# Kernel tuning notes

Measured on AMD Instinct MI355X. Metric: run time of the kernel, lower is better.

Reference implementation:

```python
import jax, jax.numpy as jnp
import numpy as np

B, S, DIN, DIM = 4, 4096, 256, 256
GAMMA = 0.9865


def setup_inputs() -> dict:
    key = jax.random.key(0)
    ks = jax.random.split(key, 9)
    inp = {
        'xq': jax.random.normal(ks[0], (B, S, DIN), dtype=jnp.float32),
        'xk': jax.random.normal(ks[1], (B, S, DIN), dtype=jnp.float32),
        'xv': jax.random.normal(ks[2], (B, S, DIN), dtype=jnp.float32),
        'Wq': jax.random.normal(ks[3], (DIN, DIM), dtype=jnp.float32) * 0.05,
        'bq': jnp.zeros((DIM,), dtype=jnp.float32),
        'Wk': jax.random.normal(ks[4], (DIN, DIM), dtype=jnp.float32) * 0.05,
        'bk': jnp.zeros((DIM,), dtype=jnp.float32),
        'Wv': jax.random.normal(ks[5], (DIN, DIM), dtype=jnp.float32) * 0.05,
        'bv': jnp.zeros((DIM,), dtype=jnp.float32),
    }
    return inp


def _decay_matrix(s, gamma):
    # D[i, j] = gamma^(i-j) if i >= j else 0
    idx = jnp.arange(s)
    diff = idx[:, None] - idx[None, :]
    D = jnp.where(diff >= 0,
                  jnp.power(jnp.float32(gamma), diff.astype(jnp.float32)),
                  jnp.float32(0.0))
    return D


def reference(xq, xk, xv, Wq, bq, Wk, bk, Wv, bv):
    Q = xq @ Wq + bq  # [B,S,D]
    K = xk @ Wk + bk  # [B,S,D]
    V = xv @ Wv + bv  # [B,S,D]
    d = Q.shape[-1]
    # scores[b,i,j] = Q[b,i] . K[b,j] / sqrt(d)
    x = jnp.einsum('bid,bjd->bij', Q, K) / jnp.sqrt(jnp.float32(d))
    D = _decay_matrix(S, GAMMA)
    # Faithful to TF broadcasting: divides along the LAST axis (per-column by
    # sqrt of that index's row-sum): D[i,j] /= sqrt(sum_k D[j,k])
    D = D / jnp.sqrt(jnp.sum(D, axis=-1))
    x = x * D  # broadcast [B,S,S] * [S,S]
    # _norm_3 per batch element with TF broadcasting: x[b,i,j] /= max(|sum_k x[b,j,k]|, 1)
    denom = jnp.maximum(jnp.abs(jnp.sum(x, axis=-1)), 1.0)  # [B,S]
    x = x / denom[:, None, :]
    return x @ V  # [B,S,D]
```

## Files before the change

### kernel.cpp

```cpp
#include <hip/hip_runtime.h>
#include <math.h>

#define BB 4
#define SS 4096
#define DD 256
#define LL 256
#define NCH 16
#define GAMMA 0.9865f
#define LOG2G (-0.019609034f)
#define INV1MG 74.07407407f
#define SLAB 1032
#define SLABB 520

typedef __attribute__((ext_vector_type(8))) short short8;
typedef __attribute__((ext_vector_type(4))) float f32x4;
typedef unsigned short u16;
typedef unsigned int u32;

__device__ __forceinline__ u16 f2bf(float f) {
  union { float f; unsigned u; } v; v.f = f;
  unsigned r = v.u + 0x7FFFu + ((v.u >> 16) & 1u);
  return (u16)(r >> 16);
}
__device__ __forceinline__ float bf2f(u16 h) {
  union { unsigned u; float f; } v; v.u = ((unsigned)h) << 16; return v.f;
}

__device__ __forceinline__ void gll16(const u16* g, u16* l) {
  __builtin_amdgcn_global_load_lds(
      (const __attribute__((address_space(1))) u32*)g,
      (__attribute__((address_space(3))) u32*)l, 16, 0, 0);
}
__device__ __forceinline__ void stage8kp(const u16* g, u16* l, int lane) {
#pragma unroll
  for (int i = 0; i < 8; ++i)
    gll16(g + i * 512 + lane * 8, l + (i >> 1) * SLAB + (i & 1) * 512);
}
__device__ __forceinline__ void stageB64(const u16* g, u16* l, int lane) {
#pragma unroll
  for (int i = 0; i < 4; ++i)
    gll16(g + i * 1024 + lane * 8, l + i * SLABB);
}
__device__ __forceinline__ void stageAB(
    const u16* AhP, const u16* AlP, const u16* BhP, const u16* BlP, int ks,
    u16* Ab, u16* Bb, int wave, int lane)
{
  if (wave == 0) stage8kp(AhP + ks * 4096, Ab, lane);
  if (wave == 1) stage8kp(AlP + ks * 4096, Ab + 4 * SLAB, lane);
  if (wave == 2) stageB64(BhP + ks * 4096, Bb, lane);
  if (wave == 3) stageB64(BlP + ks * 4096, Bb + 4 * SLABB, lane);
}

__device__ __forceinline__ void mfma_step_regB(
    const u16* Ah, const u16* Al, const short8 bh[4], const short8 bl[4],
    int wm0, int fm, int fq, f32x4 acc[4][4])
{
  const int ka = fq * SLAB;
  short8 ah[4], al[4];
#pragma unroll
  for (int i = 0; i < 4; ++i) {
    ah[i] = *(const short8*)&Ah[ka + (wm0 + i * 16 + fm) * 8];
    al[i] = *(const short8*)&Al[ka + (wm0 + i * 16 + fm) * 8];
  }
#pragma unroll
  for (int j = 0; j < 4; ++j)
#pragma unroll
    for (int i = 0; i < 4; ++i) {
      acc[i][j] = __builtin_amdgcn_mfma_f32_16x16x32_bf16(al[i], bh[j], acc[i][j], 0, 0, 0);
      acc[i][j] = __builtin_amdgcn_mfma_f32_16x16x32_bf16(ah[i], bl[j], acc[i][j], 0, 0, 0);
      acc[i][j] = __builtin_amdgcn_mfma_f32_16x16x32_bf16(ah[i], bh[j], acc[i][j], 0, 0, 0);
    }
}

__device__ __forceinline__ void loadBW(short8 bh[4], short8 bl[4],
    const u16* WhP, const u16* WlP, int ks, int wn0, int fm, int fq)
{
  const int base = ks * 4096 + fq * 1024;
#pragma unroll
  for (int j = 0; j < 4; ++j) {
    int o = base + (wn0 + j * 16 + fm) * 8;
    bh[j] = *(const short8*)&WhP[o];
    bl[j] = *(const short8*)&WlP[o];
  }
}

__device__ __forceinline__ void mfma_step_ab(
    const u16* Ah, const u16* Al, const u16* Bh, const u16* Bl,
    int wm0, int wn0, int fm, int fq, f32x4 acc[4][2])
{
  const int ka = fq * SLAB, kb = fq * SLABB;
  short8 ah[4], al[4];
#pragma unroll
  for (int i = 0; i < 4; ++i) {
    ah[i] = *(const short8*)&Ah[ka + (wm0 + i * 16 + fm) * 8];
    al[i] = *(const short8*)&Al[ka + (wm0 + i * 16 + fm) * 8];
  }
#pragma unroll
  for (int j = 0; j < 2; ++j) {
    short8 bh = *(const short8*)&Bh[kb + (wn0 + j * 16 + fm) * 8];
    short8 bl = *(const short8*)&Bl[kb + (wn0 + j * 16 + fm) * 8];
#pragma unroll
    for (int i = 0; i < 4; ++i) {
      acc[i][j] = __builtin_amdgcn_mfma_f32_16x16x32_bf16(al[i], bh, acc[i][j], 0, 0, 0);
      acc[i][j] = __builtin_amdgcn_mfma_f32_16x16x32_bf16(ah[i], bl, acc[i][j], 0, 0, 0);
      acc[i][j] = __builtin_amdgcn_mfma_f32_16x16x32_bf16(ah[i], bh, acc[i][j], 0, 0, 0);
    }
  }
}

__device__ __forceinline__ void bounce_write(
    float* fb, const f32x4 acc[4][4], int wm0, int wn0, int fm, int fq, int p)
{
  if (wn0 == p * 64) {
#pragma unroll
    for (int i = 0; i < 4; ++i)
#pragma unroll
      for (int j = 0; j < 4; ++j)
#pragma unroll
        for (int r = 0; r < 4; ++r)
          fb[(wm0 + i * 16 + fq * 4 + r) * 65 + j * 16 + fm] = acc[i][j][r];
  }
}

__global__ __launch_bounds__(256) void init_pack_kernel(
    const float* __restrict__ Wq, const float* __restrict__ Wk, const float* __restrict__ Wv,
    u16* __restrict__ Wth, u16* __restrict__ Wtl,
    float* __restrict__ rsP, float* __restrict__ lVec)
{
  const int which = blockIdx.x;
  const int it = blockIdx.y;
  const int t = threadIdx.x;
  if (which == 0) {
    *(float4*)&rsP[(size_t)(it * 256 + t) * 4] = (float4){0.f, 0.f, 0.f, 0.f};
  } else if (which == 1) {
    *(float4*)&lVec[(size_t)(it * 256 + t) * 4] = (float4){0.f, 0.f, 0.f, 0.f};
  }
  const float* W = which == 0 ? Wq : (which == 1 ? Wk : Wv);
  for (int pn = 0; pn < 2; ++pn) {
    int pos = it * 256 + t;
    int k8 = pos >> 7, r = pos & 127;
    u16 hs[8], ls[8];
#pragma unroll
    for (int u = 0; u < 8; ++u) {
      float x = W[(size_t)(k8 * 8 + u) * DD + pn * 128 + r];
      u16 h = f2bf(x); hs[u] = h; ls[u] = f2bf(x - bf2f(h));
    }
    size_t o = ((size_t)((which * 2 + pn) * 32 + k8)) * 1024 + (size_t)r * 8;
    *(short8*)&Wth[o] = *(short8*)hs;
    *(short8*)&Wtl[o] = *(short8*)ls;
  }
}

__device__ __forceinline__ void loadX(float xs[2][8], const float* XP, int ks,
                                      int arow, int ak8) {
#pragma unroll
  for (int t = 0; t < 2; ++t) {
    const float* src = XP + (size_t)(t * 64 + arow) * DD + ks * 32 + ak8 * 8;
    *(float4*)&xs[t][0] = *(const float4*)src;
    *(float4*)&xs[t][4] = *(const float4*)(src + 4);
  }
}
__device__ __forceinline__ void writeAsplit(u16* Ab, const float xs[2][8],
                                            int arow, int ak8) {
#pragma unroll
  for (int t = 0; t < 2; ++t) {
    int row = t * 64 + arow;
    u16 hs[8], ls[8];
#pragma unroll
    for (int u = 0; u < 8; ++u) {
      u16 h = f2bf(xs[t][u]); hs[u] = h; ls[u] = f2bf(xs[t][u] - bf2f(h));
    }
    *(short8*)&Ab[ak8 * SLAB + row * 8] = *(short8*)hs;
    *(short8*)&Ab[4 * SLAB + ak8 * SLAB + row * 8] = *(short8*)ls;
  }
}

__global__ __launch_bounds__(256, 3) void proj_kernel(
    const float* __restrict__ xq, const float* __restrict__ xk, const float* __restrict__ xv,
    const u16* __restrict__ Wth, const u16* __restrict__ Wtl,
    const float* __restrict__ bq, const float* __restrict__ bk_, const float* __restrict__ bv,
    u16* __restrict__ Qh, u16* __restrict__ Ql,
    u16* __restrict__ Kh, u16* __restrict__ Kl,
    u16* __restrict__ KTh, u16* __restrict__ KTl, float* __restrict__ VT32,
    float* __restrict__ lVec)
{
  const int which = blockIdx.z;
  const float* bias = which == 0 ? bq : (which == 1 ? bk_ : bv);
  const int m0 = blockIdx.x * 128;
  const int pn = blockIdx.y;
  __shared__ u16 SM[16 * SLAB + 128];
  __shared__ float rsc[128];
  __shared__ float wlut[128];
  __shared__ float kacc[64];
  float* fb = (float*)SM;
  const int tid = threadIdx.x, lane = tid & 63, wave = tid >> 6;
  const int wm0 = (wave >> 1) * 64, wn0 = (wave & 1) * 64;
  const int fm = lane & 15, fq = lane >> 4;
  if (which == 1) {
    if (tid < 128) {
      int sb = (m0 & (SS - 1)) + tid;
      rsc[tid] = rsqrtf((1.0f - exp2f((float)(sb + 1) * LOG2G)) * INV1MG);
      wlut[tid] = exp2f((float)(255 - ((m0 & (LL - 1)) + tid)) * LOG2G);
    }
    if (tid < 64) kacc[tid] = 0.f;
  }
  const float* XP = (which == 0 ? xq : (which == 1 ? xk : xv)) + (size_t)m0 * DD;
  const u16* WhP = Wth + (size_t)((which * 2 + pn) * 32) * 1024;
  const u16* WlP = Wtl + (size_t)((which * 2 + pn) * 32) * 1024;
  const int arow = tid >> 2, ak8 = tid & 3;
  f32x4 acc[4][4];
#pragma unroll
  for (int i = 0; i < 4; ++i)
#pragma unroll
    for (int j = 0; j < 4; ++j) acc[i][j] = (f32x4){0.f, 0.f, 0.f, 0.f};
  float xs[2][8];
  short8 bh[4], bl[4];
  loadBW(bh, bl, WhP, WlP, 0, wn0, fm, fq);
  loadX(xs, XP, 0, arow, ak8);
  writeAsplit(SM, xs, arow, ak8);
  int cur = 0;
  for (int ks = 0; ks < 8; ++ks) {
    __syncthreads();
    u16* Ac = SM + cur * 8 * SLAB;
    u16* An = SM + (cur ^ 1) * 8 * SLAB;
    if (ks < 7) loadX(xs, XP, ks + 1, arow, ak8);
    mfma_step_regB(Ac, Ac + 4 * SLAB, bh, bl, wm0, fm, fq, acc);
    if (ks < 7) {
      loadBW(bh, bl, WhP, WlP, ks + 1, wn0, fm, fq);
      writeAsplit(An, xs, arow, ak8);
    }
    cur ^= 1;
  }
  const int b = m0 >> 12, sbb = m0 & (SS - 1);
  for (int p = 0; p < 2; ++p) {
    __syncthreads();
    bounce_write(fb, acc, wm0, wn0, fm, fq, p);
    __syncthreads();
    if (which == 0) {
#pragma unroll
      for (int it = 0; it < 4; ++it) {
        int unit = it * 256 + tid;
        int k8l = unit >> 7, row = unit & 127;
        int gcol0 = pn * 128 + p * 64 + k8l * 8;
        u16 hs[8], ls[8];
#pragma unroll
        for (int u = 0; u < 8; ++u) {
          float v = (fb[row * 65 + k8l * 8 + u] + bias[gcol0 + u]) * (1.f / 16.f);
          u16 h = f2bf(v); hs[u] = h; ls[u] = f2bf(v - bf2f(h));
        }
        size_t o = (size_t)(m0 >> 7) * 32768 + (size_t)(pn * 16 + p * 8 + k8l) * 1024 + row * 8;
        *(short8*)&Qh[o] = *(short8*)hs;
        *(short8*)&Ql[o] = *(short8*)ls;
      }
    } else if (which == 1) {
#pragma unroll
      for (int it = 0; it < 4; ++it) {
        int unit = it * 256 + tid;
        int k8l = unit >> 7, row = unit & 127;
        int gcol0 = pn * 128 + p * 64 + k8l * 8;
        u16 hs[8], ls[8];
#pragma unroll
        for (int u = 0; u < 8; ++u) {
          float v = (fb[row * 65 + k8l * 8 + u] + bias[gcol0 + u]) * rsc[row];
          u16 h = f2bf(v); hs[u] = h; ls[u] = f2bf(v - bf2f(h));
        }
        size_t o = (size_t)(m0 >> 7) * 32768 + (size_t)(pn * 16 + p * 8 + k8l) * 1024 + row * 8;
        *(short8*)&Kh[o] = *(short8*)hs;
        *(short8*)&Kl[o] = *(short8*)ls;
      }
      float kpart = 0.f;
#pragma unroll
      for (int it = 0; it < 4; ++it) {
        int unit = it * 256 + tid;
        int dl = unit & 63, s8l = unit >> 6;
        int gcolg = pn * 128 + p * 64 + dl;
        float bs = bias[gcolg];
        u16 hs[8], ls[8];
#pragma unroll
        for (int u = 0; u < 8; ++u) {
          int row = s8l * 8 + u;
          float v = (fb[row * 65 + dl] + bs) * rsc[row];
          kpart = fmaf(v, wlut[row], kpart);
          u16 h = f2bf(v); hs[u] = h; ls[u] = f2bf(v - bf2f(h));
        }
        int sb0 = sbb + s8l * 8;
        size_t o = ((size_t)(b * 2 + (gcolg >> 7)) * 512 + (sb0 >> 3)) * 1024 + (size_t)(gcolg & 127) * 8;
        *(short8*)&KTh[o] = *(short8*)hs;
        *(short8*)&KTl[o] = *(short8*)ls;
      }
      atomicAdd(&kacc[tid & 63], kpart);
      __syncthreads();
      if (tid < 64) {
        int c = sbb >> 8;
        atomicAdd(&lVec[(size_t)(b * NCH + c) * DD + pn * 128 + p * 64 + tid], kacc[tid]);
        kacc[tid] = 0.f;
      }
    } else {
#pragma unroll
      for (int it = 0; it < 4; ++it) {
        int unit = it * 256 + tid;
        int dl = unit & 63, s8l = unit >> 6;
        int gcolg = pn * 128 + p * 64 + dl;
        float bs = bias[gcolg];
        float vv[8];
#pragma unroll
        for (int u = 0; u < 8; ++u) vv[u] = fb[(s8l * 8 + u) * 65 + dl] + bs;
        float* dst = &VT32[(size_t)b * DD * SS + (size_t)gcolg * SS + sbb + s8l * 8];
        *(float4*)dst = (float4){vv[0], vv[1], vv[2], vv[3]};
        *(float4*)(dst + 4) = (float4){vv[4], vv[5], vv[6], vv[7]};
      }
    }
  }
}

__global__ __launch_bounds__(256, 3) void scores_kernel(
    const u16* __restrict__ Qh, const u16* __restrict__ Ql,
    const u16* __restrict__ Kh, const u16* __restrict__ Kl,
    const float* __restrict__ lVec, u16* __restrict__ Sgh, u16* __restrict__ Sgl,
    float* __restrict__ rsP)
{
  const int chunk = blockIdx.x, b = chunk >> 4, c = chunk & 15;
  const int y = blockIdx.y;
  const int m0 = (y < 2) ? 0 : 128;
  const int jn0 = (y < 2) ? y * 64 : (y - 2) * 64;
  __shared__ u16 SA[2 * 8 * SLAB];
  __shared__ u16 SB[2 * 8 * SLABB];
  __shared__ float cv[256], lut[256], rowAcc[128], qd2[2][128];
  float* fb = (float*)SA;
  const int tid = threadIdx.x, lane = tid & 63, wave = tid >> 6;
  const int wm0 = (wave >> 1) * 64, wn0 = (wave & 1) * 32;
  const int fm = lane & 15, fq = lane >> 4;
  if (jn0 == 0) {
    const float gL = exp2f((float)LL * LOG2G);
    float s = 0.f;
    for (int cp = 0; cp < c; ++cp)
      s = fmaf(gL, s, lVec[(size_t)(b * NCH + cp) * DD + tid]);
    cv[tid] = s;
  }
  lut[tid] = exp2f((float)tid * LOG2G);
  if (tid < 128) rowAcc[tid] = 0.f;
  const int growA = b * SS + c * LL + m0;
  const int growB = b * SS + c * LL + jn0;
  const u16* QhP = Qh + (size_t)(growA >> 7) * 32768;
  const u16* QlP = Ql + (size_t)(growA >> 7) * 32768;
  const u16* KhP = Kh + (size_t)(growB >> 7) * 32768 + (size_t)(growB & 127) * 8;
  const u16* KlP = Kl + (size_t)(growB >> 7) * 32768 + (size_t)(growB & 127) * 8;
  f32x4 acc[4][2];
#pragma unroll
  for (int i = 0; i < 4; ++i)
#pragma unroll
    for (int j = 0; j < 2; ++j) acc[i][j] = (f32x4){0.f, 0.f, 0.f, 0.f};
  float qdreg = 0.f;
  const int qrow = tid & 127, qk8b = tid >> 7;
  stageAB(QhP, QlP, KhP, KlP, 0, SA, SB, wave, lane);
  int cur = 0;
  for (int ks = 0; ks < 8; ++ks) {
    __syncthreads();
    u16* Ac = cur ? SA + 8 * SLAB : SA;
    u16* Bc = cur ? SB + 8 * SLABB : SB;
    u16* An = cur ? SA : SA + 8 * SLAB;
    u16* Bn = cur ? SB : SB + 8 * SLABB;
    if (ks < 7) stageAB(QhP, QlP, KhP, KlP, ks + 1, An, Bn, wave, lane);
    mfma_step_ab(Ac, Ac + 4 * SLAB, Bc, Bc + 4 * SLABB, wm0, wn0, fm, fq, acc);
    if (jn0 == 0) {
#pragma unroll
      for (int h2 = 0; h2 < 2; ++h2) {
        int k8l = qk8b + 2 * h2;
        const u16* ahp = &Ac[k8l * SLAB + qrow * 8];
        const u16* alp = &Ac[4 * SLAB + k8l * SLAB + qrow * 8];
#pragma unroll
        for (int u = 0; u < 8; ++u)
          qdreg = fmaf(bf2f(ahp[u]) + bf2f(alp[u]), cv[ks * 32 + k8l * 8 + u], qdreg);
      }
    }
    cur ^= 1;
  }
  qd2[qk8b][qrow] = qdreg;
  const int ps = chunk * 2 + (m0 >> 7);
  for (int rh = 0; rh < 2; ++rh) {
    __syncthreads();
    if (wm0 == rh * 64) {
#pragma unroll
      for (int i = 0; i < 4; ++i)
#pragma unroll
        for (int j = 0; j < 2; ++j)
#pragma unroll
          for (int r = 0; r < 4; ++r)
            fb[(i * 16 + fq * 4 + r) * 65 + wn0 + j * 16 + fm] = acc[i][j][r];
    }
    __syncthreads();
#pragma unroll
    for (int it = 0; it < 2; ++it) {
      int unit = it * 256 + tid;
      int k8l = unit >> 6, rowl = unit & 63;
      int il = m0 + rh * 64 + rowl;
      int jlb = jn0 + k8l * 8;
      float part = 0.f;
      u16 hs[8], ls[8];
#pragma unroll
      for (int u = 0; u < 8; ++u) {
        int jl = jlb + u;
        float v = (jl <= il) ? fb[rowl * 65 + k8l * 8 + u] * lut[il - jl] : 0.f;
        part += v;
        u16 h = f2bf(v); hs[u] = h; ls[u] = f2bf(v - bf2f(h));
      }
      atomicAdd(&rowAcc[rh * 64 + rowl], part);
      size_t o = (size_t)(ps * 32 + (jn0 >> 3) + k8l) * 1024 + (size_t)(rh * 64 + rowl) * 8;
      *(short8*)&Sgh[o] = *(short8*)hs;
      *(short8*)&Sgl[o] = *(short8*)ls;
    }
  }
  __syncthreads();
  if (tid < 128) {
    float rs = rowAcc[tid];
    if (jn0 == 0)
      rs += exp2f((float)(m0 + tid + 1) * LOG2G) * (qd2[0][tid] + qd2[1][tid]);
    atomicAdd(&rsP[(size_t)b * SS + c * LL + m0 + tid], rs);
  }
}

__global__ __launch_bounds__(256, 3) void lmat_kernel(
    const float* __restrict__ VT32, const float* __restrict__ rsP,
    const u16* __restrict__ KTh, const u16* __restrict__ KTl,
    float* __restrict__ lMatT)
{
  const int chunk = blockIdx.x, b = chunk >> 4, c = chunk & 15;
  const int ty = blockIdx.y;
  const int m0 = (ty >> 2) * 128, n0 = (ty & 3) * 64;
  __shared__ u16 SA[2 * 8 * SLAB];
  __shared__ u16 SB[2 * 8 * SLABB];
  __shared__ float swl[256];
  const int tid = threadIdx.x, lane = tid & 63, wave = tid >> 6;
  const int wm0 = (wave >> 1) * 64, wn0 = (wave & 1) * 32;
  const int fm = lane & 15, fq = lane >> 4;
  swl[tid] = exp2f((float)(255 - tid) * LOG2G) /
             fmaxf(fabsf(rsP[(size_t)b * SS + c * LL + tid]), 1.0f);
  const float* AP = VT32 + (size_t)b * DD * SS + (size_t)m0 * SS + c * LL;
  const u16* BhP = KTh + ((size_t)(b * 2 + (n0 >> 7)) * 512 + c * 32) * 1024 + (size_t)(n0 & 127) * 8;
  const u16* BlP = KTl + ((size_t)(b * 2 + (n0 >> 7)) * 512 + c * 32) * 1024 + (size_t)(n0 & 127) * 8;
  const int arow = tid >> 1;
  f32x4 acc[4][2];
#pragma unroll
  for (int i = 0; i < 4; ++i)
#pragma unroll
    for (int j = 0; j < 2; ++j) acc[i][j] = (f32x4){0.f, 0.f, 0.f, 0.f};
  float as[2][8];
#pragma unroll
  for (int t = 0; t < 2; ++t) {
    int ak8 = (tid & 1) * 2 + t;
    const float* src = AP + (size_t)arow * SS + ak8 * 8;
    *(float4*)&as[t][0] = *(const float4*)src;
    *(float4*)&as[t][4] = *(const float4*)(src + 4);
  }
  __syncthreads();
#pragma unroll
  for (int t = 0; t < 2; ++t) {
    int ak8 = (tid & 1) * 2 + t;
    u16 hs[8], ls[8];
#pragma unroll
    for (int u = 0; u < 8; ++u) {
      float v = as[t][u] * swl[ak8 * 8 + u];
      u16 h = f2bf(v); hs[u] = h; ls[u] = f2bf(v - bf2f(h));
    }
    *(short8*)&SA[ak8 * SLAB + arow * 8] = *(short8*)hs;
    *(short8*)&SA[4 * SLAB + ak8 * SLAB + arow * 8] = *(short8*)ls;
  }
  if (wave == 2) stageB64(BhP, SB, lane);
  if (wave == 3) stageB64(BlP, SB + 4 * SLABB, lane);
  int cur = 0;
  for (int ks = 0; ks < 8; ++ks) {
    __syncthreads();
    u16* Ac = cur ? SA + 8 * SLAB : SA;
    u16* Bc = cur ? SB + 8 * SLABB : SB;
    u16* An = cur ? SA : SA + 8 * SLAB;
    u16* Bn = cur ? SB : SB + 8 * SLABB;
    if (ks < 7) {
#pragma unroll
      for (int t = 0; t < 2; ++t) {
        int ak8 = (tid & 1) * 2 + t;
        const float* src = AP + (size_t)arow * SS + (ks + 1) * 32 + ak8 * 8;
        *(float4*)&as[t][0] = *(const float4*)src;
        *(float4*)&as[t][4] = *(const float4*)(src + 4);
      }
      if (wave == 2) stageB64(BhP + (ks + 1) * 4096, Bn, lane);
      if (wave == 3) stageB64(BlP + (ks + 1) * 4096, Bn + 4 * SLABB, lane);
    }
    mfma_step_ab(Ac, Ac + 4 * SLAB, Bc, Bc + 4 * SLABB, wm0, wn0, fm, fq, acc);
    if (ks < 7) {
#pragma unroll
      for (int t = 0; t < 2; ++t) {
        int ak8 = (tid & 1) * 2 + t;
        u16 hs[8], ls[8];
#pragma unroll
        for (int u = 0; u < 8; ++u) {
          float v = as[t][u] * swl[(ks + 1) * 32 + ak8 * 8 + u];
          u16 h = f2bf(v); hs[u] = h; ls[u] = f2bf(v - bf2f(h));
        }
        *(short8*)&An[ak8 * SLAB + arow * 8] = *(short8*)hs;
        *(short8*)&An[4 * SLAB + ak8 * SLAB + arow * 8] = *(short8*)ls;
      }
    }
    cur ^= 1;
  }
#pragma unroll
  for (int i = 0; i < 4; ++i)
#pragma unroll
    for (int j = 0; j < 2; ++j)
#pragma unroll
      for (int r = 0; r < 4; ++r) {
        int e = m0 + wm0 + i * 16 + fq * 4 + r;
        int d = n0 + wn0 + j * 16 + fm;
        lMatT[(size_t)chunk * 65536 + (size_t)e * 256 + d] = acc[i][j][r];
      }
}

__global__ __launch_bounds__(256) void combine_mat_kernel(
    const float* __restrict__ lMatT, u16* __restrict__ cMh, u16* __restrict__ cMl)
{
  const int t = blockIdx.x * 256 + threadIdx.x;
  const int b = t >> 13, rem = t & 8191;
  const int k8 = rem >> 8, e = rem & 255;
  const float gL = powf(GAMMA, (float)LL);
  float s[8] = {0.f, 0.f, 0.f, 0.f, 0.f, 0.f, 0.f, 0.f};
  for (int ch = 0; ch < 16; ++ch) {
    size_t ro = (size_t)(b * 16 + ch) * 65536 + (size_t)e * 256 + k8 * 8;
    float4 a0 = *(const float4*)&lMatT[ro];
    float4 a1 = *(const float4*)&lMatT[ro + 4];
    float vals[8] = {a0.x, a0.y, a0.z, a0.w, a1.x, a1.y, a1.z, a1.w};
    u16 hh[8], ll[8];
#pragma unroll
    for (int u = 0; u < 8; ++u) {
      u16 h = f2bf(s[u]); hh[u] = h; ll[u] = f2bf(s[u] - bf2f(h));
    }
    size_t wo = ((size_t)(((b * 16 + ch) * 2 + (e >> 7)) * 32 + k8)) * 1024 + (size_t)(e & 127) * 8;
    *(short8*)&cMh[wo] = *(short8*)hh;
    *(short8*)&cMl[wo] = *(short8*)ll;
#pragma unroll
    for (int u = 0; u < 8; ++u) s[u] = gL * s[u] + vals[u];
  }
}

__global__ __launch_bounds__(256, 3) void out_kernel(
    const u16* __restrict__ Qh, const u16* __restrict__ Ql,
    const u16* __restrict__ cMh, const u16* __restrict__ cMl,
    const u16* __restrict__ Sgh, const u16* __restrict__ Sgl,
    const float* __restrict__ VT32, const float* __restrict__ rsP,
    float* __restrict__ out)
{
  const int chunk = blockIdx.x, b = chunk >> 4, c = chunk & 15;
  const int ty = blockIdx.y;
  const int m0 = (ty >> 2) * 128, n0 = (ty & 3) * 64;
  __shared__ u16 SA[2 * 8 * SLAB];
  __shared__ u16 SB[2 * 8 * SLABB];
  __shared__ float olut[128];
  __shared__ float sdn[256];
  const int tid = threadIdx.x, lane = tid & 63, wave = tid >> 6;
  const int wm0 = (wave >> 1) * 64, wn0 = (wave & 1) * 32;
  const int fm = lane & 15, fq = lane >> 4;
  if (tid < 128) olut[tid] = exp2f((float)(m0 + tid + 1) * LOG2G);
  sdn[tid] = 1.0f / fmaxf(fabsf(rsP[(size_t)b * SS + c * LL + tid]), 1.0f);
  f32x4 acc[4][2];
#pragma unroll
  for (int i = 0; i < 4; ++i)
#pragma unroll
    for (int j = 0; j < 2; ++j) acc[i][j] = (f32x4){0.f, 0.f, 0.f, 0.f};
  int cur = 0;
  {
    const u16* AhP = Qh + (size_t)(b * 32 + c * 2 + (m0 >> 7)) * 32768;
    const u16* AlP = Ql + (size_t)(b * 32 + c * 2 + (m0 >> 7)) * 32768;
    const u16* BhP = cMh + (size_t)(chunk * 2 + (n0 >> 7)) * 32768 + (size_t)(n0 & 127) * 8;
    const u16* BlP = cMl + (size_t)(chunk * 2 + (n0 >> 7)) * 32768 + (size_t)(n0 & 127) * 8;
    stageAB(AhP, AlP, BhP, BlP, 0, SA, SB, wave, lane);
    for (int ks = 0; ks < 8; ++ks) {
      __syncthreads();
      u16* Ac = cur ? SA + 8 * SLAB : SA;
      u16* Bc = cur ? SB + 8 * SLABB : SB;
      u16* An = cur ? SA : SA + 8 * SLAB;
      u16* Bn = cur ? SB : SB + 8 * SLABB;
      if (ks < 7) stageAB(AhP, AlP, BhP, BlP, ks + 1, An, Bn, wave, lane);
      mfma_step_ab(Ac, Ac + 4 * SLAB, Bc, Bc + 4 * SLABB, wm0, wn0, fm, fq, acc);
      cur ^= 1;
    }
  }
  {
    const u16* AhP = Sgh + (size_t)(chunk * 2 + (m0 >> 7)) * 32768;
    const u16* AlP = Sgl + (size_t)(chunk * 2 + (m0 >> 7)) * 32768;
    const float* BP = VT32 + (size_t)b * DD * SS + (size_t)n0 * SS + c * LL;
    const int ber = tid >> 2, bk8 = tid & 3;
    const int nks = (m0 >> 5) + 4;
    float bs[8];
    {
      u16* Ac = cur ? SA + 8 * SLAB : SA;
      u16* Bc = cur ? SB + 8 * SLABB : SB;
      if (wave == 0) stage8kp(AhP, Ac, lane);
      if (wave == 1) stage8kp(AlP, Ac + 4 * SLAB, lane);
      const float* src = BP + (size_t)ber * SS + bk8 * 8;
      *(float4*)&bs[0] = *(const float4*)src;
      *(float4*)&bs[4] = *(const float4*)(src + 4);
#pragma unroll
      for (int i = 0; i < 4; ++i)
#pragma unroll
        for (int r = 0; r < 4; ++r) {
          int rl = wm0 + i * 16 + fq * 4 + r;
          float sc = olut[rl];
#pragma unroll
          for (int j = 0; j < 2; ++j) acc[i][j][r] *= sc;
        }
      u16 hs[8], ls[8];
#pragma unroll
      for (int u = 0; u < 8; ++u) {
        float v = bs[u] * sdn[bk8 * 8 + u];
        u16 h = f2bf(v); hs[u] = h; ls[u] = f2bf(v - bf2f(h));
      }
      *(short8*)&Bc[bk8 * SLABB + ber * 8] = *(short8*)hs;
      *(short8*)&Bc[4 * SLABB + bk8 * SLABB + ber * 8] = *(short8*)ls;
    }
    for (int ks = 0; ks < nks; ++ks) {
      __syncthreads();
      u16* Ac = cur ? SA + 8 * SLAB : SA;
      u16* Bc = cur ? SB + 8 * SLABB : SB;
      u16* An = cur ? SA : SA + 8 * SLAB;
      u16* Bn = cur ? SB : SB + 8 * SLABB;
      if (ks + 1 < nks) {
        if (wave == 0) stage8kp(AhP + (ks + 1) * 4096, An, lane);
        if (wave == 1) stage8kp(AlP + (ks + 1) * 4096, An + 4 * SLAB, lane);
        const float* src = BP + (size_t)ber * SS + (ks + 1) * 32 + bk8 * 8;
        *(float4*)&bs[0] = *(const float4*)src;
        *(float4*)&bs[4] = *(const float4*)(src + 4);
      }
      mfma_step_ab(Ac, Ac + 4 * SLAB, Bc, Bc + 4 * SLABB, wm0, wn0, fm, fq, acc);
      if (ks + 1 < nks) {
        u16 hs[8], ls[8];
#pragma unroll
        for (int u = 0; u < 8; ++u) {
          float v = bs[u] * sdn[(ks + 1) * 32 + bk8 * 8 + u];
          u16 h = f2bf(v); hs[u] = h; ls[u] = f2bf(v - bf2f(h));
        }
        *(short8*)&Bn[bk8 * SLABB + ber * 8] = *(short8*)hs;
        *(short8*)&Bn[4 * SLABB + bk8 * SLABB + ber * 8] = *(short8*)ls;
      }
      cur ^= 1;
    }
  }
#pragma unroll
  for (int i = 0; i < 4; ++i)
#pragma unroll
    for (int j = 0; j < 2; ++j)
#pragma unroll
      for (int r = 0; r < 4; ++r) {
        int il = m0 + wm0 + i * 16 + fq * 4 + r;
        int e = n0 + wn0 + j * 16 + fm;
        out[(size_t)(b * SS + c * LL + il) * DD + e] = acc[i][j][r];
      }
}

extern "C" void kernel_launch(void* const* d_in, const int* in_sizes, int n_in,
                              void* d_out, int out_size, void* d_ws, size_t ws_size,
                              hipStream_t stream) {
  const float* xq = (const float*)d_in[0];
  const float* xk = (const float*)d_in[1];
  const float* xv = (const float*)d_in[2];
  const float* Wq = (const float*)d_in[3];
  const float* bq = (const float*)d_in[4];
  const float* Wk = (const float*)d_in[5];
  const float* bk = (const float*)d_in[6];
  const float* Wv = (const float*)d_in[7];
  const float* bv = (const float*)d_in[8];
  float* out = (float*)d_out;

  char* p = (char*)d_ws;
  const size_t H16 = (size_t)BB * SS * DD * 2;
  u16* Qh   = (u16*)(p + 0 * H16);  u16* Ql   = (u16*)(p + 1 * H16);
  u16* Kh   = (u16*)(p + 2 * H16);  u16* Kl   = (u16*)(p + 3 * H16);
  u16* KTh  = (u16*)(p + 4 * H16);  u16* KTl  = (u16*)(p + 5 * H16);
  u16* Sgh  = (u16*)(p + 10 * H16); u16* Sgl  = (u16*)(p + 11 * H16);
  u16* cMh  = (u16*)(p + 12 * H16); u16* cMl  = (u16*)(p + 13 * H16);
  float* lMatT = (float*)(p + 14 * H16);
  float* VT32  = (float*)(p + 16 * H16);
  u16* Wth = (u16*)(p + 18 * H16);
  u16* Wtl = (u16*)(p + 18 * H16 + 3 * DD * DD * 2);
  float* rsP  = (float*)(p + 18 * H16 + 6 * DD * DD * 2);
  float* lVec = rsP + (size_t)BB * SS;

  init_pack_kernel<<<dim3(3, 16), 256, 0, stream>>>(Wq, Wk, Wv, Wth, Wtl, rsP, lVec);
  proj_kernel<<<dim3(BB * SS / 128, 2, 3), 256, 0, stream>>>(
      xq, xk, xv, Wth, Wtl, bq, bk, bv, Qh, Ql, Kh, Kl, KTh, KTl, VT32, lVec);
  scores_kernel<<<dim3(BB * NCH, 6), 256, 0, stream>>>(
      Qh, Ql, Kh, Kl, lVec, Sgh, Sgl, rsP);
  lmat_kernel<<<dim3(BB * NCH, 8), 256, 0, stream>>>(VT32, rsP, KTh, KTl, lMatT);
  combine_mat_kernel<<<128, 256, 0, stream>>>(lMatT, cMh, cMl);
  out_kernel<<<dim3(BB * NCH, 8), 256, 0, stream>>>(
      Qh, Ql, cMh, cMl, Sgh, Sgl, VT32, rsP, out);
}
```

Before: 202.1 us.

## Load B operand directly into registers instead of staging through LDS

In the scores, lmat and output kernels, the B-side (K / cM / KT) bf16 hi/lo fragments are now read straight from global memory into registers, one k-step ahead, instead of being staged into a double-buffered shared-memory tile. This removes the SB shared buffer and its LDS traffic, and launch bounds are raised from 3 to 4 blocks per CU to use the freed LDS. The trade-off is that each wave issues its own uncoalesced-ish global loads for B, and register pressure rises, which may cause spills under the tighter occupancy bound.

```diff
diff --git a/kernel.cpp b/kernel.cpp
--- a/kernel.cpp
+++ b/kernel.cpp
@@ -36,20 +36,6 @@
   for (int i = 0; i < 8; ++i)
     gll16(g + i * 512 + lane * 8, l + (i >> 1) * SLAB + (i & 1) * 512);
 }
-__device__ __forceinline__ void stageB64(const u16* g, u16* l, int lane) {
-#pragma unroll
-  for (int i = 0; i < 4; ++i)
-    gll16(g + i * 1024 + lane * 8, l + i * SLABB);
-}
-__device__ __forceinline__ void stageAB(
-    const u16* AhP, const u16* AlP, const u16* BhP, const u16* BlP, int ks,
-    u16* Ab, u16* Bb, int wave, int lane)
-{
-  if (wave == 0) stage8kp(AhP + ks * 4096, Ab, lane);
-  if (wave == 1) stage8kp(AlP + ks * 4096, Ab + 4 * SLAB, lane);
-  if (wave == 2) stageB64(BhP + ks * 4096, Bb, lane);
-  if (wave == 3) stageB64(BlP + ks * 4096, Bb + 4 * SLABB, lane);
-}
 
 __device__ __forceinline__ void mfma_step_regB(
     const u16* Ah, const u16* Al, const short8 bh[4], const short8 bl[4],
@@ -72,6 +58,27 @@
     }
 }
 
+__device__ __forceinline__ void mfma_step_regB_ab(
+    const u16* Ah, const u16* Al, const short8 bh[2], const short8 bl[2],
+    int wm0, int fm, int fq, f32x4 acc[4][2])
+{
+  const int ka = fq * SLAB;
+  short8 ah[4], al[4];
+#pragma unroll
+  for (int i = 0; i < 4; ++i) {
+    ah[i] = *(const short8*)&Ah[ka + (wm0 + i * 16 + fm) * 8];
+    al[i] = *(const short8*)&Al[ka + (wm0 + i * 16 + fm) * 8];
+  }
+#pragma unroll
+  for (int j = 0; j < 2; ++j)
+#pragma unroll
+    for (int i = 0; i < 4; ++i) {
+      acc[i][j] = __builtin_amdgcn_mfma_f32_16x16x32_bf16(al[i], bh[j], acc[i][j], 0, 0, 0);
+      acc[i][j] = __builtin_amdgcn_mfma_f32_16x16x32_bf16(ah[i], bl[j], acc[i][j], 0, 0, 0);
+      acc[i][j] = __builtin_amdgcn_mfma_f32_16x16x32_bf16(ah[i], bh[j], acc[i][j], 0, 0, 0);
+    }
+}
+
 __device__ __forceinline__ void loadBW(short8 bh[4], short8 bl[4],
     const u16* WhP, const u16* WlP, int ks, int wn0, int fm, int fq)
 {
@@ -81,6 +88,17 @@
     int o = base + (wn0 + j * 16 + fm) * 8;
     bh[j] = *(const short8*)&WhP[o];
     bl[j] = *(const short8*)&WlP[o];
+  }
+}
+__device__ __forceinline__ void loadB2(short8 bh[2], short8 bl[2],
+    const u16* BhP, const u16* BlP, int ks, int wn0, int fm, int fq)
+{
+  const int base = ks * 4096 + fq * 1024;
+#pragma unroll
+  for (int j = 0; j < 2; ++j) {
+    int o = base + (wn0 + j * 16 + fm) * 8;
+    bh[j] = *(const short8*)&BhP[o];
+    bl[j] = *(const short8*)&BlP[o];
   }
 }
 
@@ -313,7 +331,7 @@
   }
 }
 
-__global__ __launch_bounds__(256, 3) void scores_kernel(
+__global__ __launch_bounds__(256, 4) void scores_kernel(
     const u16* __restrict__ Qh, const u16* __restrict__ Ql,
     const u16* __restrict__ Kh, const u16* __restrict__ Kl,
     const float* __restrict__ lVec, u16* __restrict__ Sgh, u16* __restrict__ Sgl,
@@ -324,7 +342,6 @@
   const int m0 = (y < 2) ? 0 : 128;
   const int jn0 = (y < 2) ? y * 64 : (y - 2) * 64;
   __shared__ u16 SA[2 * 8 * SLAB];
-  __shared__ u16 SB[2 * 8 * SLABB];
   __shared__ float cv[256], lut[256], rowAcc[128], qd2[2][128];
   float* fb = (float*)SA;
   const int tid = threadIdx.x, lane = tid & 63, wave = tid >> 6;
@@ -352,16 +369,21 @@
     for (int j = 0; j < 2; ++j) acc[i][j] = (f32x4){0.f, 0.f, 0.f, 0.f};
   float qdreg = 0.f;
   const int qrow = tid & 127, qk8b = tid >> 7;
-  stageAB(QhP, QlP, KhP, KlP, 0, SA, SB, wave, lane);
+  short8 bh[2], bl[2];
+  if (wave == 0) stage8kp(QhP, SA, lane);
+  if (wave == 1) stage8kp(QlP, SA + 4 * SLAB, lane);
+  loadB2(bh, bl, KhP, KlP, 0, wn0, fm, fq);
   int cur = 0;
   for (int ks = 0; ks < 8; ++ks) {
     __syncthreads();
     u16* Ac = cur ? SA + 8 * SLAB : SA;
-    u16* Bc = cur ? SB + 8 * SLABB : SB;
     u16* An = cur ? SA : SA + 8 * SLAB;
-    u16* Bn = cur ? SB : SB + 8 * SLABB;
-    if (ks < 7) stageAB(QhP, QlP, KhP, KlP, ks + 1, An, Bn, wave, lane);
-    mfma_step_ab(Ac, Ac + 4 * SLAB, Bc, Bc + 4 * SLABB, wm0, wn0, fm, fq, acc);
+    if (ks < 7) {
+      if (wave == 0) stage8kp(QhP + (ks + 1) * 4096, An, lane);
+      if (wave == 1) stage8kp(QlP + (ks + 1) * 4096, An + 4 * SLAB, lane);
+    }
+    mfma_step_regB_ab(Ac, Ac + 4 * SLAB, bh, bl, wm0, fm, fq, acc);
+    if (ks < 7) loadB2(bh, bl, KhP, KlP, ks + 1, wn0, fm, fq);
     if (jn0 == 0) {
 #pragma unroll
       for (int h2 = 0; h2 < 2; ++h2) {
@@ -419,7 +441,7 @@
   }
 }
 
-__global__ __launch_bounds__(256, 3) void lmat_kernel(
+__global__ __launch_bounds__(256, 4) void lmat_kernel(
     const float* __restrict__ VT32, const float* __restrict__ rsP,
     const u16* __restrict__ KTh, const u16* __restrict__ KTl,
     float* __restrict__ lMatT)
@@ -428,7 +450,6 @@
   const int ty = blockIdx.y;
   const int m0 = (ty >> 2) * 128, n0 = (ty & 3) * 64;
   __shared__ u16 SA[2 * 8 * SLAB];
-  __shared__ u16 SB[2 * 8 * SLABB];
   __shared__ float swl[256];
   const int tid = threadIdx.x, lane = tid & 63, wave = tid >> 6;
   const int wm0 = (wave >> 1) * 64, wn0 = (wave & 1) * 32;
@@ -445,6 +466,8 @@
 #pragma unroll
     for (int j = 0; j < 2; ++j) acc[i][j] = (f32x4){0.f, 0.f, 0.f, 0.f};
   float as[2][8];
+  short8 bh[2], bl[2];
+  loadB2(bh, bl, BhP, BlP, 0, wn0, fm, fq);
 #pragma unroll
   for (int t = 0; t < 2; ++t) {
     int ak8 = (tid & 1) * 2 + t;
@@ -465,15 +488,11 @@
     *(short8*)&SA[ak8 * SLAB + arow * 8] = *(short8*)hs;
     *(short8*)&SA[4 * SLAB + ak8 * SLAB + arow * 8] = *(short8*)ls;
   }
-  if (wave == 2) stageB64(BhP, SB, lane);
-  if (wave == 3) stageB64(BlP, SB + 4 * SLABB, lane);
   int cur = 0;
   for (int ks = 0; ks < 8; ++ks) {
     __syncthreads();
     u16* Ac = cur ? SA + 8 * SLAB : SA;
-    u16* Bc = cur ? SB + 8 * SLABB : SB;
     u16* An = cur ? SA : SA + 8 * SLAB;
-    u16* Bn = cur ? SB : SB + 8 * SLABB;
     if (ks < 7) {
 #pragma unroll
       for (int t = 0; t < 2; ++t) {
@@ -482,11 +501,10 @@
         *(float4*)&as[t][0] = *(const float4*)src;
         *(float4*)&as[t][4] = *(const float4*)(src + 4);
       }
-      if (wave == 2) stageB64(BhP + (ks + 1) * 4096, Bn, lane);
-      if (wave == 3) stageB64(BlP + (ks + 1) * 4096, Bn + 4 * SLABB, lane);
-    }
-    mfma_step_ab(Ac, Ac + 4 * SLAB, Bc, Bc + 4 * SLABB, wm0, wn0, fm, fq, acc);
+    }
+    mfma_step_regB_ab(Ac, Ac + 4 * SLAB, bh, bl, wm0, fm, fq, acc);
     if (ks < 7) {
+      loadB2(bh, bl, BhP, BlP, ks + 1, wn0, fm, fq);
 #pragma unroll
       for (int t = 0; t < 2; ++t) {
         int ak8 = (tid & 1) * 2 + t;
@@ -570,15 +588,20 @@
     const u16* AlP = Ql + (size_t)(b * 32 + c * 2 + (m0 >> 7)) * 32768;
     const u16* BhP = cMh + (size_t)(chunk * 2 + (n0 >> 7)) * 32768 + (size_t)(n0 & 127) * 8;
     const u16* BlP = cMl + (size_t)(chunk * 2 + (n0 >> 7)) * 32768 + (size_t)(n0 & 127) * 8;
-    stageAB(AhP, AlP, BhP, BlP, 0, SA, SB, wave, lane);
+    short8 bh[2], bl[2];
+    if (wave == 0) stage8kp(AhP, SA, lane);
+    if (wave == 1) stage8kp(AlP, SA + 4 * SLAB, lane);
+    loadB2(bh, bl, BhP, BlP, 0, wn0, fm, fq);
     for (int ks = 0; ks < 8; ++ks) {
       __syncthreads();
       u16* Ac = cur ? SA + 8 * SLAB : SA;
-      u16* Bc = cur ? SB + 8 * SLABB : SB;
       u16* An = cur ? SA : SA + 8 * SLAB;
-      u16* Bn = cur ? SB : SB + 8 * SLABB;
-      if (ks < 7) stageAB(AhP, AlP, BhP, BlP, ks + 1, An, Bn, wave, lane);
-      mfma_step_ab(Ac, Ac + 4 * SLAB, Bc, Bc + 4 * SLABB, wm0, wn0, fm, fq, acc);
+      if (ks < 7) {
+        if (wave == 0) stage8kp(AhP + (ks + 1) * 4096, An, lane);
+        if (wave == 1) stage8kp(AlP + (ks + 1) * 4096, An + 4 * SLAB, lane);
+      }
+      mfma_step_regB_ab(Ac, Ac + 4 * SLAB, bh, bl, wm0, fm, fq, acc);
+      if (ks < 7) loadB2(bh, bl, BhP, BlP, ks + 1, wn0, fm, fq);
       cur ^= 1;
     }
   }
```

Result: faster. 198.2 us (-2.0%).
